# Performance work log

Measured on AMD Instinct MI355X. Metric: run time of the kernel, lower is better.

The kernel has to match this reference:

```python
import jax, jax.numpy as jnp
import numpy as np

B, N, D, H, M, NN, K = 2, 2048, 256, 8, 2, 2048, 8


def setup_inputs() -> dict:
    key = jax.random.key(0)
    ks = jax.random.split(key, 8)
    s = 0.02
    return {
        "current_points": jax.random.normal(ks[0], (B, N, 3), jnp.float32),
        "current_features": jax.random.normal(ks[1], (B, N, D), jnp.float32),
        "neighbor_points": jax.random.normal(ks[2], (M, B, NN, 3), jnp.float32),
        "neighbor_features": jax.random.normal(ks[3], (M, B, NN, D), jnp.float32),
        "in_proj_w": jax.random.normal(ks[4], (3 * D, D), jnp.float32) * s,
        "in_proj_b": jnp.zeros((3 * D,), jnp.float32),
        "out_proj_w": jax.random.normal(ks[5], (D, D), jnp.float32) * s,
        "out_proj_b": jnp.zeros((D,), jnp.float32),
        "spatial_w": jax.random.normal(ks[6], (D, 3), jnp.float32) * s,
        "spatial_b": jnp.zeros((D,), jnp.float32),
    }


def _knn_edge_features(points, features, k):
    # points [b,n,3], features [b,n,d] -> edge features [b,n,d]
    sq = jnp.sum(points * points, axis=-1)                       # [b,n]
    d2 = sq[:, :, None] + sq[:, None, :] - 2.0 * jnp.einsum('bnc,bmc->bnm', points, points)
    _, idx = jax.lax.top_k(-d2, k)                               # k nearest (incl. self), [b,n,k]
    b_idx = jnp.arange(points.shape[0])[:, None, None]
    nbr = features[b_idx, idx]                                   # gather neighbor feats [b,n,k,d]
    return features - jnp.mean(nbr, axis=2)


def _mha(q, kv, in_w, in_b, out_w, out_b, h):
    # torch nn.MultiheadAttention (batch_first) cross-attention
    d = q.shape[-1]
    dh = d // h
    wq, wk, wv = jnp.split(in_w, 3, axis=0)
    bq, bk, bv = jnp.split(in_b, 3, axis=0)
    qp = q @ wq.T + bq                                           # [b,Lq,d]
    kp = kv @ wk.T + bk                                          # [b,Lk,d]
    vp = kv @ wv.T + bv

    def heads(x):
        b, l, _ = x.shape
        return x.reshape(b, l, h, dh).transpose(0, 2, 1, 3)      # [b,h,l,dh]

    qh, kh, vh = heads(qp), heads(kp), heads(vp)
    scores = jnp.einsum('bhqd,bhkd->bhqk', qh, kh) / np.sqrt(dh).astype(np.float32)
    attn = jax.nn.softmax(scores, axis=-1)
    o = jnp.einsum('bhqk,bhkd->bhqd', attn, vh)
    b, _, lq, _ = o.shape
    o = o.transpose(0, 2, 1, 3).reshape(b, lq, d)
    return o @ out_w.T + out_b


def reference(current_points, current_features, neighbor_points, neighbor_features,
              in_proj_w, in_proj_b, out_proj_w, out_proj_b, spatial_w, spatial_b):
    cur_edge = _knn_edge_features(current_points, current_features, K)       # [B,N,D]
    nbr_edge = jax.vmap(lambda p, f: _knn_edge_features(p, f, K))(neighbor_points, neighbor_features)  # [M,B,NN,D]
    all_nbr = jnp.transpose(nbr_edge, (1, 0, 2, 3)).reshape(B, M * NN, D)    # cat along seq dim
    aligned = _mha(cur_edge, all_nbr, in_proj_w, in_proj_b, out_proj_w, out_proj_b, H)
    spatial = current_points @ spatial_w.T + spatial_b                       # [B,N,D]
    return aligned + spatial
```

## Files before the change

### kernel.cpp

```cpp
#include <hip/hip_runtime.h>
#include <hip/hip_bf16.h>

typedef __bf16 bf16_t;
typedef __attribute__((ext_vector_type(8))) __bf16 bf16x8;
typedef __attribute__((ext_vector_type(4))) __bf16 bf16x4;
typedef __attribute__((ext_vector_type(4))) float f32x4;


__global__ __launch_bounds__(256) void wconv_kernel(const float* __restrict__ w_in,
                                                    const float* __restrict__ w_out,
                                                    bf16_t* __restrict__ w_in_b,
                                                    bf16_t* __restrict__ w_out_b) {
    int i = blockIdx.x * 256 + threadIdx.x;
    if (i < 768 * 256) w_in_b[i] = (bf16_t)w_in[i];
    if (i < 256 * 256) w_out_b[i] = (bf16_t)w_out[i];
}

__global__ __launch_bounds__(1024) void knn_kernel(const float* __restrict__ cur_pts,
                                                   const float* __restrict__ nbr_pts,
                                                   int* __restrict__ idx_out) {
    int p = blockIdx.y;
    const float* pts = (p < 2) ? (cur_pts + (size_t)p * 2048 * 3)
                               : (nbr_pts + (size_t)(p - 2) * 2048 * 3);

    __shared__ __align__(16) float4 spts[2048];

    int tid = threadIdx.x;
    for (int i = tid; i < 2048; i += 1024) {
        float x = pts[i * 3 + 0], y = pts[i * 3 + 1], z = pts[i * 3 + 2];
        float sq = __fadd_rn(__fadd_rn(__fmul_rn(x, x), __fmul_rn(y, y)), __fmul_rn(z, z));
        spts[i] = make_float4(x, y, z, sq);
    }
    __syncthreads();

    int wave = tid >> 6, lane = tid & 63;
    int q = blockIdx.x * 16 + wave;
    float4 qp4 = spts[q];

    float dist[8];
    int di[8];
#pragma unroll
    for (int r = 0; r < 8; r++) { dist[r] = 3.4e38f; di[r] = 0x7fffffff; }

    for (int t = 0; t < 32; t++) {
        int j = t * 64 + lane;
        float4 pp = spts[j];
        float dot = __fadd_rn(__fadd_rn(__fmul_rn(qp4.x, pp.x), __fmul_rn(qp4.y, pp.y)),
                              __fmul_rn(qp4.z, pp.z));
        float d2 = __fsub_rn(__fadd_rn(qp4.w, pp.w), __fmul_rn(2.0f, dot));
        if (d2 < dist[7]) {
#pragma unroll
            for (int r = 7; r >= 1; --r) {
                bool cm = d2 < dist[r - 1];
                bool cr = d2 < dist[r];
                float nd = cm ? dist[r - 1] : (cr ? d2 : dist[r]);
                int ni = cm ? di[r - 1] : (cr ? j : di[r]);
                dist[r] = nd; di[r] = ni;
            }
            if (d2 < dist[0]) { dist[0] = d2; di[0] = j; }
        }
    }

    int res[8];
#pragma unroll
    for (int r = 0; r < 8; r++) {
        float bd = dist[0];
        int bi = di[0];
#pragma unroll
        for (int m = 1; m < 64; m <<= 1) {
            float od = __shfl_xor(bd, m);
            int oi = __shfl_xor(bi, m);
            if (od < bd || (od == bd && oi < bi)) { bd = od; bi = oi; }
        }
        res[r] = bi;
        bool win = (di[0] == bi);
#pragma unroll
        for (int k = 0; k < 7; k++) {
            dist[k] = win ? dist[k + 1] : dist[k];
            di[k]   = win ? di[k + 1]   : di[k];
        }
        if (win) { dist[7] = 3.4e38f; di[7] = 0x7fffffff; }
    }

    if (lane == 0) {
        int4* o = (int4*)(idx_out + ((size_t)p * 2048 + q) * 8);
        o[0] = make_int4(res[0], res[1], res[2], res[3]);
        o[1] = make_int4(res[4], res[5], res[6], res[7]);
    }
}

__global__ __launch_bounds__(64) void edge_kernel(const float* __restrict__ cur_feat,
                                                  const float* __restrict__ nbr_feat,
                                                  const int* __restrict__ idx_buf,
                                                  bf16_t* __restrict__ cur_edge,
                                                  bf16_t* __restrict__ all_nbr) {
    int blk = blockIdx.x;
    int p = blk >> 11, q = blk & 2047;
    const float* feat;
    bf16_t* outp;
    if (p < 2) {
        feat = cur_feat + (size_t)p * 2048 * 256;
        outp = cur_edge + ((size_t)p * 2048 + q) * 256;
    } else {
        int mb = p - 2;
        int m = mb >> 1, bb = mb & 1;
        feat = nbr_feat + (size_t)mb * 2048 * 256;
        outp = all_nbr + ((size_t)bb * 4096 + m * 2048 + q) * 256;
    }
    const int* idx = idx_buf + ((size_t)p * 2048 + q) * 8;
    int t = threadIdx.x;
    float4 self = ((const float4*)(feat + (size_t)q * 256))[t];
    float sx = 0.f, sy = 0.f, sz = 0.f, sw = 0.f;
#pragma unroll
    for (int r = 0; r < 8; r++) {
        float4 f = ((const float4*)(feat + (size_t)idx[r] * 256))[t];
        sx += f.x; sy += f.y; sz += f.z; sw += f.w;
    }
    bf16x4 v;
    v[0] = (bf16_t)(self.x - sx * 0.125f);
    v[1] = (bf16_t)(self.y - sy * 0.125f);
    v[2] = (bf16_t)(self.z - sz * 0.125f);
    v[3] = (bf16_t)(self.w - sw * 0.125f);
    *(bf16x4*)(outp + 4 * t) = v;
}

__global__ __launch_bounds__(256) void qkv_kernel(const bf16_t* __restrict__ cur_edge,
                                                  const bf16_t* __restrict__ all_nbr,
                                                  const bf16_t* __restrict__ w_in,
                                                  const float* __restrict__ b_in,
                                                  bf16_t* __restrict__ qp,
                                                  bf16_t* __restrict__ kp,
                                                  bf16_t* __restrict__ vpT) {
    int z = blockIdx.z;
    int Mrows = (z == 0) ? 4096 : 8192;
    int m0base = blockIdx.y * 64;
    if (m0base >= Mrows) return;
    const bf16_t* A = (z == 0) ? cur_edge : all_nbr;
    const bf16_t* W = w_in + (size_t)z * 256 * 256;

    int wave = threadIdx.x >> 6, lane = threadIdx.x & 63;
    int wr = wave >> 1, wc = wave & 1;
    int m0 = m0base + wr * 32;
    int n0 = blockIdx.x * 64 + wc * 32;
    int lr = lane & 15, lg = lane >> 4;

    f32x4 acc[2][2] = {};
    for (int kc = 0; kc < 256; kc += 32) {
        bf16x8 a[2], b[2];
#pragma unroll
        for (int i = 0; i < 2; i++)
            a[i] = *(const bf16x8*)(A + (size_t)(m0 + i * 16 + lr) * 256 + kc + lg * 8);
#pragma unroll
        for (int i = 0; i < 2; i++)
            b[i] = *(const bf16x8*)(W + (size_t)(n0 + i * 16 + lr) * 256 + kc + lg * 8);
#pragma unroll
        for (int i = 0; i < 2; i++)
#pragma unroll
            for (int j = 0; j < 2; j++)
                acc[i][j] = __builtin_amdgcn_mfma_f32_16x16x32_bf16(a[i], b[j], acc[i][j], 0, 0, 0);
    }

    const float inv_s = 0.17677669529663687f;
#pragma unroll
    for (int i = 0; i < 2; i++)
#pragma unroll
        for (int j = 0; j < 2; j++)
#pragma unroll
            for (int r = 0; r < 4; r++) {
                int mm = m0 + i * 16 + lg * 4 + r;
                int nn = n0 + j * 16 + lr;
                float v = acc[i][j][r] + b_in[z * 256 + nn];
                if (z == 0) {
                    qp[(size_t)mm * 256 + nn] = (bf16_t)(v * inv_s);
                } else if (z == 1) {
                    kp[(size_t)mm * 256 + nn] = (bf16_t)v;
                } else {
                    int bb = mm >> 12, kv = mm & 4095, h = nn >> 5, dd = nn & 31;
                    vpT[(((size_t)bb * 8 + h) * 32 + dd) * 4096 + kv] = (bf16_t)v;
                }
            }
}

__global__ __launch_bounds__(256) void attn_kernel(const bf16_t* __restrict__ qp,
                                                   const bf16_t* __restrict__ kp,
                                                   const bf16_t* __restrict__ vpT,
                                                   bf16_t* __restrict__ o_buf) {
    int bh = blockIdx.y;
    int b = bh >> 3, h = bh & 7;
    int wave = threadIdx.x >> 6, lane = threadIdx.x & 63;
    int lr = lane & 15, lg = lane >> 4;
    int q0 = blockIdx.x * 128 + wave * 32;

    const bf16_t* Qb = qp + ((size_t)b * 2048 + q0) * 256 + h * 32;
    const bf16_t* Kb = kp + (size_t)b * 4096 * 256 + h * 32;
    const bf16_t* Vb = vpT + ((size_t)b * 8 + h) * 32 * 4096;

    __shared__ __align__(16) bf16_t P_lds[4][2][16][32];

    bf16x8 qfrag[2];
    qfrag[0] = *(const bf16x8*)(Qb + (size_t)lr * 256 + lg * 8);
    qfrag[1] = *(const bf16x8*)(Qb + (size_t)(16 + lr) * 256 + lg * 8);

    f32x4 oacc[2][2] = {};
    float lsum[2][4] = {};
    const f32x4 zf = {0.f, 0.f, 0.f, 0.f};

    for (int kv0 = 0; kv0 < 4096; kv0 += 32) {
        bf16x8 kfrag[2];
        kfrag[0] = *(const bf16x8*)(Kb + (size_t)(kv0 + lr) * 256 + lg * 8);
        kfrag[1] = *(const bf16x8*)(Kb + (size_t)(kv0 + 16 + lr) * 256 + lg * 8);

#pragma unroll
        for (int ms = 0; ms < 2; ms++) {
            f32x4 s0 = __builtin_amdgcn_mfma_f32_16x16x32_bf16(qfrag[ms], kfrag[0], zf, 0, 0, 0);
            f32x4 s1 = __builtin_amdgcn_mfma_f32_16x16x32_bf16(qfrag[ms], kfrag[1], zf, 0, 0, 0);
#pragma unroll
            for (int r = 0; r < 4; r++) {
                float p0 = __expf(s0[r]);
                float p1 = __expf(s1[r]);
                lsum[ms][r] += p0 + p1;
                P_lds[wave][ms][lg * 4 + r][lr] = (bf16_t)p0;
                P_lds[wave][ms][lg * 4 + r][16 + lr] = (bf16_t)p1;
            }
        }

        bf16x8 vfrag[2];
        vfrag[0] = *(const bf16x8*)(Vb + (size_t)lr * 4096 + kv0 + lg * 8);
        vfrag[1] = *(const bf16x8*)(Vb + (size_t)(16 + lr) * 4096 + kv0 + lg * 8);

#pragma unroll
        for (int ms = 0; ms < 2; ms++) {
            bf16x8 pf = *(const bf16x8*)(&P_lds[wave][ms][lr][lg * 8]);
            oacc[ms][0] = __builtin_amdgcn_mfma_f32_16x16x32_bf16(pf, vfrag[0], oacc[ms][0], 0, 0, 0);
            oacc[ms][1] = __builtin_amdgcn_mfma_f32_16x16x32_bf16(pf, vfrag[1], oacc[ms][1], 0, 0, 0);
        }
    }

#pragma unroll
    for (int ms = 0; ms < 2; ms++)
#pragma unroll
        for (int r = 0; r < 4; r++) {
            float s = lsum[ms][r];
            s += __shfl_xor(s, 1);
            s += __shfl_xor(s, 2);
            s += __shfl_xor(s, 4);
            s += __shfl_xor(s, 8);
            lsum[ms][r] = s;
        }

#pragma unroll
    for (int ms = 0; ms < 2; ms++)
#pragma unroll
        for (int ds = 0; ds < 2; ds++)
#pragma unroll
            for (int r = 0; r < 4; r++) {
                float v = oacc[ms][ds][r] / lsum[ms][r];
                int qq = q0 + ms * 16 + lg * 4 + r;
                int dd = h * 32 + ds * 16 + lr;
                o_buf[((size_t)b * 2048 + qq) * 256 + dd] = (bf16_t)v;
            }
}

__global__ __launch_bounds__(256) void outproj_kernel(const bf16_t* __restrict__ o_buf,
                                                      const bf16_t* __restrict__ w_out,
                                                      const float* __restrict__ b_out,
                                                      const float* __restrict__ cur_pts,
                                                      const float* __restrict__ sw,
                                                      const float* __restrict__ sb,
                                                      float* __restrict__ out) {
    int wave = threadIdx.x >> 6, lane = threadIdx.x & 63;
    int wr = wave >> 1, wc = wave & 1;
    int m0 = blockIdx.y * 64 + wr * 32;
    int n0 = blockIdx.x * 64 + wc * 32;
    int lr = lane & 15, lg = lane >> 4;

    f32x4 acc[2][2] = {};
    for (int kc = 0; kc < 256; kc += 32) {
        bf16x8 a[2], b[2];
#pragma unroll
        for (int i = 0; i < 2; i++)
            a[i] = *(const bf16x8*)(o_buf + (size_t)(m0 + i * 16 + lr) * 256 + kc + lg * 8);
#pragma unroll
        for (int i = 0; i < 2; i++)
            b[i] = *(const bf16x8*)(w_out + (size_t)(n0 + i * 16 + lr) * 256 + kc + lg * 8);
#pragma unroll
        for (int i = 0; i < 2; i++)
#pragma unroll
            for (int j = 0; j < 2; j++)
                acc[i][j] = __builtin_amdgcn_mfma_f32_16x16x32_bf16(a[i], b[j], acc[i][j], 0, 0, 0);
    }

#pragma unroll
    for (int i = 0; i < 2; i++)
#pragma unroll
        for (int j = 0; j < 2; j++)
#pragma unroll
            for (int r = 0; r < 4; r++) {
                int mm = m0 + i * 16 + lg * 4 + r;
                int nn = n0 + j * 16 + lr;
                const float* pp = cur_pts + (size_t)mm * 3;
                float sp = pp[0] * sw[nn * 3 + 0] + pp[1] * sw[nn * 3 + 1] + pp[2] * sw[nn * 3 + 2] + sb[nn];
                out[(size_t)mm * 256 + nn] = acc[i][j][r] + b_out[nn] + sp;
            }
}

extern "C" void kernel_launch(void* const* d_in, const int* in_sizes, int n_in,
                              void* d_out, int out_size, void* d_ws, size_t ws_size,
                              hipStream_t stream) {
    const float* cur_pts  = (const float*)d_in[0];
    const float* cur_feat = (const float*)d_in[1];
    const float* nbr_pts  = (const float*)d_in[2];
    const float* nbr_feat = (const float*)d_in[3];
    const float* in_w     = (const float*)d_in[4];
    const float* in_b     = (const float*)d_in[5];
    const float* out_w    = (const float*)d_in[6];
    const float* out_b    = (const float*)d_in[7];
    const float* sw       = (const float*)d_in[8];
    const float* sb       = (const float*)d_in[9];

    char* ws = (char*)d_ws;
    bf16_t* w_in_b  = (bf16_t*)(ws + 0);
    bf16_t* w_out_b = (bf16_t*)(ws + 393216);
    int*    idx_buf = (int*)(ws + 524288);
    bf16_t* cur_edge = (bf16_t*)(ws + 917504);
    bf16_t* all_nbr  = (bf16_t*)(ws + 3014656);
    bf16_t* qp  = (bf16_t*)(ws + 7208960);
    bf16_t* kp  = (bf16_t*)(ws + 9306112);
    bf16_t* vpT = (bf16_t*)(ws + 13500416);
    bf16_t* o_buf = (bf16_t*)(ws + 17694720);
    float* outp = (float*)d_out;

    wconv_kernel<<<dim3(768), dim3(256), 0, stream>>>(in_w, out_w, w_in_b, w_out_b);
    knn_kernel<<<dim3(128, 6), dim3(1024), 0, stream>>>(cur_pts, nbr_pts, idx_buf);
    edge_kernel<<<dim3(12288), dim3(64), 0, stream>>>(cur_feat, nbr_feat, idx_buf, cur_edge, all_nbr);
    qkv_kernel<<<dim3(4, 128, 3), dim3(256), 0, stream>>>(cur_edge, all_nbr, w_in_b, in_b, qp, kp, vpT);
    attn_kernel<<<dim3(16, 16), dim3(256), 0, stream>>>(qp, kp, vpT, o_buf);
    outproj_kernel<<<dim3(4, 64), dim3(256), 0, stream>>>(o_buf, w_out_b, out_b, cur_pts, sw, sb, outp);
}
```

Before: 244.8 us.

## Restructure attention kernel with 16-row waves, double-buffered KV loads, swizzled LDS

Each wave in the attention kernel now handles 16 query rows instead of 32, and the grid doubles to 512 blocks to raise parallelism across CUs. The KV loop steps 64 keys per compute stage and double-buffers K/V register fragments (A/B) so global loads overlap with MFMA and exp work. The P tile in LDS gets an XOR swizzle to avoid bank conflicts, and the final normalization multiplies by a reciprocal instead of dividing. In exchange, each Q row reuses K/V less, so total K/V global traffic doubles, and the larger register footprint may lower occupancy.

```diff
diff --git a/kernel.cpp b/kernel.cpp
--- a/kernel.cpp
+++ b/kernel.cpp
@@ -189,76 +189,96 @@
     int b = bh >> 3, h = bh & 7;
     int wave = threadIdx.x >> 6, lane = threadIdx.x & 63;
     int lr = lane & 15, lg = lane >> 4;
-    int q0 = blockIdx.x * 128 + wave * 32;
+    int q0 = blockIdx.x * 64 + wave * 16;
 
     const bf16_t* Qb = qp + ((size_t)b * 2048 + q0) * 256 + h * 32;
     const bf16_t* Kb = kp + (size_t)b * 4096 * 256 + h * 32;
     const bf16_t* Vb = vpT + ((size_t)b * 8 + h) * 32 * 4096;
 
-    __shared__ __align__(16) bf16_t P_lds[4][2][16][32];
-
-    bf16x8 qfrag[2];
-    qfrag[0] = *(const bf16x8*)(Qb + (size_t)lr * 256 + lg * 8);
-    qfrag[1] = *(const bf16x8*)(Qb + (size_t)(16 + lr) * 256 + lg * 8);
-
-    f32x4 oacc[2][2] = {};
-    float lsum[2][4] = {};
+    __shared__ __align__(16) char P_lds[4][16 * 128];
+    char* Pw = &P_lds[wave][0];
+
+    bf16x8 qfrag = *(const bf16x8*)(Qb + (size_t)lr * 256 + lg * 8);
+
+    f32x4 oacc[2] = {};
+    float lsum[4] = {};
     const f32x4 zf = {0.f, 0.f, 0.f, 0.f};
 
-    for (int kv0 = 0; kv0 < 4096; kv0 += 32) {
-        bf16x8 kfrag[2];
-        kfrag[0] = *(const bf16x8*)(Kb + (size_t)(kv0 + lr) * 256 + lg * 8);
-        kfrag[1] = *(const bf16x8*)(Kb + (size_t)(kv0 + 16 + lr) * 256 + lg * 8);
-
-#pragma unroll
-        for (int ms = 0; ms < 2; ms++) {
-            f32x4 s0 = __builtin_amdgcn_mfma_f32_16x16x32_bf16(qfrag[ms], kfrag[0], zf, 0, 0, 0);
-            f32x4 s1 = __builtin_amdgcn_mfma_f32_16x16x32_bf16(qfrag[ms], kfrag[1], zf, 0, 0, 0);
-#pragma unroll
-            for (int r = 0; r < 4; r++) {
-                float p0 = __expf(s0[r]);
-                float p1 = __expf(s1[r]);
-                lsum[ms][r] += p0 + p1;
-                P_lds[wave][ms][lg * 4 + r][lr] = (bf16_t)p0;
-                P_lds[wave][ms][lg * 4 + r][16 + lr] = (bf16_t)p1;
-            }
+    const bf16_t* Kp0 = Kb + (size_t)lr * 256 + lg * 8;
+    const bf16_t* Vp0 = Vb + (size_t)lr * 4096 + lg * 8;
+
+    bf16x8 kfA[4], vfA[4], kfB[4], vfB[4];
+
+#define LOADKV(KF, VF, KV0)                                                   \
+    {                                                                         \
+        _Pragma("unroll")                                                     \
+        for (int f = 0; f < 4; f++)                                           \
+            KF[f] = *(const bf16x8*)(Kp0 + (size_t)((KV0) + f * 16) * 256);   \
+        _Pragma("unroll")                                                     \
+        for (int k = 0; k < 2; k++) {                                         \
+            VF[k]     = *(const bf16x8*)(Vp0 + (KV0) + k * 32);               \
+            VF[k + 2] = *(const bf16x8*)(Vp0 + 16 * 4096 + (KV0) + k * 32);   \
+        }                                                                     \
+    }
+
+#define COMPUTE(KF, VF)                                                       \
+    {                                                                         \
+        f32x4 s[4];                                                           \
+        _Pragma("unroll")                                                     \
+        for (int f = 0; f < 4; f++)                                           \
+            s[f] = __builtin_amdgcn_mfma_f32_16x16x32_bf16(qfrag, KF[f], zf, 0, 0, 0); \
+        _Pragma("unroll")                                                     \
+        for (int f = 0; f < 4; f++) {                                         \
+            _Pragma("unroll")                                                 \
+            for (int r = 0; r < 4; r++) {                                     \
+                float pv = __expf(s[f][r]);                                   \
+                lsum[r] += pv;                                                \
+                int qrow = lg * 4 + r;                                        \
+                int cb = (f * 32 + 2 * lr) ^ ((qrow & 7) << 4);               \
+                *(bf16_t*)(Pw + qrow * 128 + cb) = (bf16_t)pv;                \
+            }                                                                 \
+        }                                                                     \
+        bf16x8 pf[2];                                                         \
+        _Pragma("unroll")                                                     \
+        for (int k = 0; k < 2; k++)                                           \
+            pf[k] = *(bf16x8*)(Pw + lr * 128 + ((k * 64 + lg * 16) ^ ((lr & 7) << 4))); \
+        _Pragma("unroll")                                                     \
+        for (int nf = 0; nf < 2; nf++) {                                      \
+            _Pragma("unroll")                                                 \
+            for (int k = 0; k < 2; k++)                                       \
+                oacc[nf] = __builtin_amdgcn_mfma_f32_16x16x32_bf16(pf[k], VF[nf * 2 + k], oacc[nf], 0, 0, 0); \
+        }                                                                     \
+    }
+
+    LOADKV(kfA, vfA, 0)
+    for (int kv0 = 0; kv0 < 4096; kv0 += 128) {
+        LOADKV(kfB, vfB, kv0 + 64)
+        COMPUTE(kfA, vfA)
+        if (kv0 + 128 < 4096) { LOADKV(kfA, vfA, kv0 + 128) }
+        COMPUTE(kfB, vfB)
+    }
+#undef LOADKV
+#undef COMPUTE
+
+#pragma unroll
+    for (int r = 0; r < 4; r++) {
+        float s = lsum[r];
+        s += __shfl_xor(s, 1);
+        s += __shfl_xor(s, 2);
+        s += __shfl_xor(s, 4);
+        s += __shfl_xor(s, 8);
+        lsum[r] = 1.0f / s;
+    }
+
+#pragma unroll
+    for (int nf = 0; nf < 2; nf++)
+#pragma unroll
+        for (int r = 0; r < 4; r++) {
+            float v = oacc[nf][r] * lsum[r];
+            int qq = q0 + lg * 4 + r;
+            int dd = h * 32 + nf * 16 + lr;
+            o_buf[((size_t)b * 2048 + qq) * 256 + dd] = (bf16_t)v;
         }
-
-        bf16x8 vfrag[2];
-        vfrag[0] = *(const bf16x8*)(Vb + (size_t)lr * 4096 + kv0 + lg * 8);
-        vfrag[1] = *(const bf16x8*)(Vb + (size_t)(16 + lr) * 4096 + kv0 + lg * 8);
-
-#pragma unroll
-        for (int ms = 0; ms < 2; ms++) {
-            bf16x8 pf = *(const bf16x8*)(&P_lds[wave][ms][lr][lg * 8]);
-            oacc[ms][0] = __builtin_amdgcn_mfma_f32_16x16x32_bf16(pf, vfrag[0], oacc[ms][0], 0, 0, 0);
-            oacc[ms][1] = __builtin_amdgcn_mfma_f32_16x16x32_bf16(pf, vfrag[1], oacc[ms][1], 0, 0, 0);
-        }
-    }
-
-#pragma unroll
-    for (int ms = 0; ms < 2; ms++)
-#pragma unroll
-        for (int r = 0; r < 4; r++) {
-            float s = lsum[ms][r];
-            s += __shfl_xor(s, 1);
-            s += __shfl_xor(s, 2);
-            s += __shfl_xor(s, 4);
-            s += __shfl_xor(s, 8);
-            lsum[ms][r] = s;
-        }
-
-#pragma unroll
-    for (int ms = 0; ms < 2; ms++)
-#pragma unroll
-        for (int ds = 0; ds < 2; ds++)
-#pragma unroll
-            for (int r = 0; r < 4; r++) {
-                float v = oacc[ms][ds][r] / lsum[ms][r];
-                int qq = q0 + ms * 16 + lg * 4 + r;
-                int dd = h * 32 + ds * 16 + lr;
-                o_buf[((size_t)b * 2048 + qq) * 256 + dd] = (bf16_t)v;
-            }
 }
 
 __global__ __launch_bounds__(256) void outproj_kernel(const bf16_t* __restrict__ o_buf,
@@ -334,6 +354,6 @@
     knn_kernel<<<dim3(128, 6), dim3(1024), 0, stream>>>(cur_pts, nbr_pts, idx_buf);
     edge_kernel<<<dim3(12288), dim3(64), 0, stream>>>(cur_feat, nbr_feat, idx_buf, cur_edge, all_nbr);
     qkv_kernel<<<dim3(4, 128, 3), dim3(256), 0, stream>>>(cur_edge, all_nbr, w_in_b, in_b, qp, kp, vpT);
-    attn_kernel<<<dim3(16, 16), dim3(256), 0, stream>>>(qp, kp, vpT, o_buf);
+    attn_kernel<<<dim3(32, 16), dim3(256), 0, stream>>>(qp, kp, vpT, o_buf);
     outproj_kernel<<<dim3(4, 64), dim3(256), 0, stream>>>(o_buf, w_out_b, out_b, cur_pts, sw, sb, outp);
 }
```

Result: slower. 271.0 us (+10.7%).

## Split attention over KV chunks with a separate combine kernel

Applied to the files above, without the earlier changes.

The attention kernel now splits the 4096-long key/value range into four chunks along a new grid dimension. Each chunk writes unnormalized partial outputs (bf16) and row sums to workspace, and a new combine kernel adds them and normalizes. This raises the block count from 256 to 1024 so the GPU's many compute units are better filled, at the cost of an extra launch and partial-result traffic. Because no max subtraction is done, the partial sums can be added directly. Storing the partials in bf16 adds a small rounding step.

```diff
diff --git a/kernel.cpp b/kernel.cpp
--- a/kernel.cpp
+++ b/kernel.cpp
@@ -184,9 +184,11 @@
 __global__ __launch_bounds__(256) void attn_kernel(const bf16_t* __restrict__ qp,
                                                    const bf16_t* __restrict__ kp,
                                                    const bf16_t* __restrict__ vpT,
-                                                   bf16_t* __restrict__ o_buf) {
+                                                   bf16_t* __restrict__ Opart,
+                                                   float* __restrict__ Lpart) {
     int bh = blockIdx.y;
     int b = bh >> 3, h = bh & 7;
+    int c = blockIdx.z;
     int wave = threadIdx.x >> 6, lane = threadIdx.x & 63;
     int lr = lane & 15, lg = lane >> 4;
     int q0 = blockIdx.x * 128 + wave * 32;
@@ -205,7 +207,8 @@
     float lsum[2][4] = {};
     const f32x4 zf = {0.f, 0.f, 0.f, 0.f};
 
-    for (int kv0 = 0; kv0 < 4096; kv0 += 32) {
+    int kv_lo = c * 1024, kv_hi = kv_lo + 1024;
+    for (int kv0 = kv_lo; kv0 < kv_hi; kv0 += 32) {
         bf16x8 kfrag[2];
         kfrag[0] = *(const bf16x8*)(Kb + (size_t)(kv0 + lr) * 256 + lg * 8);
         kfrag[1] = *(const bf16x8*)(Kb + (size_t)(kv0 + 16 + lr) * 256 + lg * 8);
@@ -251,14 +254,40 @@
 #pragma unroll
     for (int ms = 0; ms < 2; ms++)
 #pragma unroll
-        for (int ds = 0; ds < 2; ds++)
-#pragma unroll
-            for (int r = 0; r < 4; r++) {
-                float v = oacc[ms][ds][r] / lsum[ms][r];
-                int qq = q0 + ms * 16 + lg * 4 + r;
+        for (int r = 0; r < 4; r++) {
+            int qq = q0 + ms * 16 + lg * 4 + r;
+            if (lr == 0)
+                Lpart[(((size_t)c * 2 + b) * 8 + h) * 2048 + qq] = lsum[ms][r];
+#pragma unroll
+            for (int ds = 0; ds < 2; ds++) {
                 int dd = h * 32 + ds * 16 + lr;
-                o_buf[((size_t)b * 2048 + qq) * 256 + dd] = (bf16_t)v;
-            }
+                Opart[(((size_t)c * 2 + b) * 2048 + qq) * 256 + dd] = (bf16_t)oacc[ms][ds][r];
+            }
+        }
+}
+
+__global__ __launch_bounds__(256) void attn_combine(const bf16_t* __restrict__ Opart,
+                                                    const float* __restrict__ Lpart,
+                                                    bf16_t* __restrict__ o_buf) {
+    int t = blockIdx.x * 256 + threadIdx.x;
+    int row = t >> 5;
+    int c8 = (t & 31) * 8;
+    int b = row >> 11, q = row & 2047, h = c8 >> 5;
+
+    float acc[8] = {};
+    float l = 0.f;
+#pragma unroll
+    for (int c = 0; c < 4; c++) {
+        bf16x8 v = *(const bf16x8*)(Opart + (((size_t)c * 2 + b) * 2048 + q) * 256 + c8);
+#pragma unroll
+        for (int j = 0; j < 8; j++) acc[j] += (float)v[j];
+        l += Lpart[(((size_t)c * 2 + b) * 8 + h) * 2048 + q];
+    }
+    float rl = 1.0f / l;
+    bf16x8 o;
+#pragma unroll
+    for (int j = 0; j < 8; j++) o[j] = (bf16_t)(acc[j] * rl);
+    *(bf16x8*)(o_buf + (size_t)row * 256 + c8) = o;
 }
 
 __global__ __launch_bounds__(256) void outproj_kernel(const bf16_t* __restrict__ o_buf,
@@ -328,12 +357,15 @@
     bf16_t* kp  = (bf16_t*)(ws + 9306112);
     bf16_t* vpT = (bf16_t*)(ws + 13500416);
     bf16_t* o_buf = (bf16_t*)(ws + 17694720);
+    bf16_t* Opart = (bf16_t*)(ws + 19791872);
+    float*  Lpart = (float*)(ws + 28180480);
     float* outp = (float*)d_out;
 
     wconv_kernel<<<dim3(768), dim3(256), 0, stream>>>(in_w, out_w, w_in_b, w_out_b);
     knn_kernel<<<dim3(128, 6), dim3(1024), 0, stream>>>(cur_pts, nbr_pts, idx_buf);
     edge_kernel<<<dim3(12288), dim3(64), 0, stream>>>(cur_feat, nbr_feat, idx_buf, cur_edge, all_nbr);
     qkv_kernel<<<dim3(4, 128, 3), dim3(256), 0, stream>>>(cur_edge, all_nbr, w_in_b, in_b, qp, kp, vpT);
-    attn_kernel<<<dim3(16, 16), dim3(256), 0, stream>>>(qp, kp, vpT, o_buf);
+    attn_kernel<<<dim3(16, 16, 4), dim3(256), 0, stream>>>(qp, kp, vpT, Opart, Lpart);
+    attn_combine<<<dim3(512), dim3(256), 0, stream>>>(Opart, Lpart, o_buf);
     outproj_kernel<<<dim3(4, 64), dim3(256), 0, stream>>>(o_buf, w_out_b, out_b, cur_pts, sw, sb, outp);
 }
```

New measurement: 221.3 us. -9.6%, faster.
